# Kernel optimization log

Measured on AMD Instinct MI355X. Metric: run time of the kernel, lower is better.

Reference implementation:

```python
import jax, jax.numpy as jnp
import numpy as np
from jax import lax

PATCH = 7
SIGMA = 12.0


def _pairwise_patch_dist_sq(A, B, p):
    # A: (Na, C, H, W), B: (Nb, C, H, W)
    # squared diff of every image pair, summed over channels -> (Na, Nb, H, W)
    diff_sq = ((A[:, None] - B[None, :]) ** 2).sum(axis=2)
    Na, Nb, H, W = diff_sq.shape
    x = diff_sq.reshape(Na * Nb, 1, H, W)
    k = jnp.ones((1, 1, p, p), dtype=x.dtype)  # box filter == conv2d with ones kernel
    d = lax.conv_general_dilated(x, k, window_strides=(1, 1), padding='VALID')
    return d.reshape(Na, Nb, H - p + 1, W - p + 1)


def _kernel_mean(d_sq, sigma, exclude_diagonal):
    K = jnp.exp(-d_sq / (2.0 * sigma ** 2))  # Gaussian RBF on squared distances
    K_pair = K.mean(axis=(-2, -1))            # (Na, Nb)
    if exclude_diagonal:
        n = K_pair.shape[0]
        off = jnp.float32(1.0) - jnp.eye(n, dtype=K_pair.dtype)
        return (K_pair * off).sum() / (n * (n - 1))
    return K_pair.mean()


def setup_inputs() -> dict:
    key = jax.random.key(0)
    kx, ky = jax.random.split(key)
    x = jax.random.normal(kx, (64, 3, 64, 64), dtype=jnp.float32)
    y = jax.random.normal(ky, (64, 3, 64, 64), dtype=jnp.float32)
    return {"x": x, "y": y}


def reference(x, y):
    d_xx = _pairwise_patch_dist_sq(x, x, PATCH)
    d_yy = _pairwise_patch_dist_sq(y, y, PATCH)
    d_xy = _pairwise_patch_dist_sq(x, y, PATCH)
    return (_kernel_mean(d_xx, SIGMA, True)
            - 2.0 * _kernel_mean(d_xy, SIGMA, False)
            + _kernel_mean(d_yy, SIGMA, True))
```

## Files before the change

kernel.cpp:

```cpp
#include <hip/hip_runtime.h>

#define NIMG 64
#define CH 3
#define WW 64
#define PLANE 4096
#define IMGSZ (CH * PLANE)
#define HO 58
#define WO 58
#define NSLOT 64

#define DS 68
#define HS 68
#define DOFF 0
#define HOFF (64 * DS)

__global__ __launch_bounds__(256) void patchmmd_pair_kernel(
    const float* __restrict__ x, const float* __restrict__ y,
    double* __restrict__ acc)
{
    const int i = blockIdx.x, j = blockIdx.y, z = blockIdx.z;
    if (z < 2 && i >= j) return;

    const float* __restrict__ A = ((z == 1) ? y : x) + (size_t)i * IMGSZ;
    const float* __restrict__ B = ((z == 0) ? x : y) + (size_t)j * IMGSZ;

    __shared__ __align__(16) float lds[HOFF + 64 * HS + 16];

    const int tid = threadIdx.x;

    #pragma unroll
    for (int t = 0; t < 4; ++t) {
        const int v = tid + t * 256;
        const int r = v >> 4, q = v & 15;
        const int off = r * WW + q * 4;
        float4 d = make_float4(0.f, 0.f, 0.f, 0.f);
        #pragma unroll
        for (int ch = 0; ch < CH; ++ch) {
            const float4 av = *reinterpret_cast<const float4*>(A + ch * PLANE + off);
            const float4 bv = *reinterpret_cast<const float4*>(B + ch * PLANE + off);
            const float ex = av.x - bv.x, ey = av.y - bv.y,
                        ez = av.z - bv.z, ew = av.w - bv.w;
            d.x = fmaf(ex, ex, d.x); d.y = fmaf(ey, ey, d.y);
            d.z = fmaf(ez, ez, d.z); d.w = fmaf(ew, ew, d.w);
        }
        *reinterpret_cast<float4*>(&lds[DOFF + r * DS + q * 4]) = d;
    }
    __syncthreads();

    #pragma unroll
    for (int t = 0; t < 2; ++t) {
        const int v = tid + t * 256;
        const int r = v >> 3, s = v & 7;
        const float* src = &lds[DOFF + r * DS + s * 8];
        const float4 q0 = *reinterpret_cast<const float4*>(src);
        const float4 q1 = *reinterpret_cast<const float4*>(src + 4);
        const float4 q2 = *reinterpret_cast<const float4*>(src + 8);
        const float4 q3 = *reinterpret_cast<const float4*>(src + 12);
        const float d0=q0.x,d1=q0.y,d2=q0.z,d3=q0.w, d4=q1.x,d5=q1.y,d6=q1.z,d7=q1.w,
                    d8=q2.x,d9=q2.y,d10=q2.z,d11=q2.w, d12=q3.x,d13=q3.y;
        float h0 = d0+d1+d2+d3+d4+d5+d6;
        const float h1 = h0 + d7  - d0;
        const float h2 = h1 + d8  - d1;
        const float h3 = h2 + d9  - d2;
        const float h4 = h3 + d10 - d3;
        const float h5 = h4 + d11 - d4;
        const float h6 = h5 + d12 - d5;
        const float h7 = h6 + d13 - d6;
        float* dst = &lds[HOFF + r * HS + s * 8];
        *reinterpret_cast<float4*>(dst)     = make_float4(h0, h1, h2, h3);
        *reinterpret_cast<float4*>(dst + 4) = make_float4(h4, h5, h6, h7);
    }
    __syncthreads();

    const float NEG_INV_2S2 = -1.0f / 288.0f;
    float local = 0.f;
    #pragma unroll
    for (int t = 0; t < 2; ++t) {
        const int v = tid + t * 256;
        const int c = v & 63;
        const int g = v >> 6;
        float hr[14];
        #pragma unroll
        for (int k = 0; k < 14; ++k) {
            const int rk = min(8 * g + k, 63);
            hr[k] = lds[HOFF + rk * HS + c];
        }
        float V = hr[0]+hr[1]+hr[2]+hr[3]+hr[4]+hr[5]+hr[6];
        #pragma unroll
        for (int jj = 0; jj < 8; ++jj) {
            if (jj > 0) V += hr[jj + 6] - hr[jj - 1];
            if ((8 * g + jj) < HO && c < WO)
                local += __expf(V * NEG_INV_2S2);
        }
    }

    #pragma unroll
    for (int off = 32; off; off >>= 1)
        local += __shfl_down(local, off, 64);
    __syncthreads();
    if ((tid & 63) == 0) lds[tid >> 6] = local;
    __syncthreads();
    if (tid == 0) {
        const float tot = lds[0] + lds[1] + lds[2] + lds[3];
        const int slot = z * NSLOT + ((i ^ (j * 19)) & (NSLOT - 1));
        atomicAdd(&acc[slot], (double)tot);
    }
}

__global__ void patchmmd_combine_kernel(const double* __restrict__ acc,
                                        float* __restrict__ out)
{
    double s[3] = {0.0, 0.0, 0.0};
    for (int z = 0; z < 3; ++z)
        for (int k = 0; k < NSLOT; ++k) s[z] += acc[z * NSLOT + k];
    const double inv_hw = 1.0 / (double)(HO * WO);
    const double mean_xx = 2.0 * s[0] * inv_hw / (64.0 * 63.0);
    const double mean_yy = 2.0 * s[1] * inv_hw / (64.0 * 63.0);
    const double mean_xy = s[2] * inv_hw / (64.0 * 64.0);
    out[0] = (float)(mean_xx - 2.0 * mean_xy + mean_yy);
}

extern "C" void kernel_launch(void* const* d_in, const int* in_sizes, int n_in,
                              void* d_out, int out_size, void* d_ws, size_t ws_size,
                              hipStream_t stream)
{
    const float* x = (const float*)d_in[0];
    const float* y = (const float*)d_in[1];
    float* out  = (float*)d_out;
    double* acc = (double*)d_ws;

    hipMemsetAsync(acc, 0, 3 * NSLOT * sizeof(double), stream);

    dim3 grid(NIMG, NIMG, 3);
    patchmmd_pair_kernel<<<grid, 256, 0, stream>>>(x, y, acc);
    patchmmd_combine_kernel<<<1, 1, 0, stream>>>(acc, out);
}
```

Baseline: 96.31 us.

## Fuse diff-square and horizontal box sum in registers, parallelize combine reduction

Each thread now loads 16 contiguous columns of one row for all channels and computes the squared differences and the horizontal 7-wide sliding sum in registers. It fetches the 6 neighbour values it needs from the adjacent lane with shuffles, which removes the intermediate LDS buffer and one barrier. The final combine kernel now runs with 64 threads and reduces with wavefront shuffles instead of a serial loop. The trade-offs are higher register pressure and less coalesced global loads, since each thread reads strided float4 chunks.

```diff
diff --git a/kernel.cpp b/kernel.cpp
--- a/kernel.cpp
+++ b/kernel.cpp
@@ -8,11 +8,7 @@
 #define HO 58
 #define WO 58
 #define NSLOT 64
-
-#define DS 68
 #define HS 68
-#define DOFF 0
-#define HOFF (64 * DS)
 
 __global__ __launch_bounds__(256) void patchmmd_pair_kernel(
     const float* __restrict__ x, const float* __restrict__ y,
@@ -24,51 +20,73 @@
     const float* __restrict__ A = ((z == 1) ? y : x) + (size_t)i * IMGSZ;
     const float* __restrict__ B = ((z == 0) ? x : y) + (size_t)j * IMGSZ;
 
-    __shared__ __align__(16) float lds[HOFF + 64 * HS + 16];
+    __shared__ __align__(16) float Hs[64 * HS + 16];
+    __shared__ float wsum[4];
 
     const int tid = threadIdx.x;
 
-    #pragma unroll
-    for (int t = 0; t < 4; ++t) {
-        const int v = tid + t * 256;
-        const int r = v >> 4, q = v & 15;
-        const int off = r * WW + q * 4;
-        float4 d = make_float4(0.f, 0.f, 0.f, 0.f);
+    {
+        const int r = tid >> 2;
+        const int s = tid & 3;
+        const int c0 = s * 16;
+        const int base = r * WW + c0;
+
+        float4 qa[6], qb[6];
         #pragma unroll
         for (int ch = 0; ch < CH; ++ch) {
-            const float4 av = *reinterpret_cast<const float4*>(A + ch * PLANE + off);
-            const float4 bv = *reinterpret_cast<const float4*>(B + ch * PLANE + off);
-            const float ex = av.x - bv.x, ey = av.y - bv.y,
-                        ez = av.z - bv.z, ew = av.w - bv.w;
-            d.x = fmaf(ex, ex, d.x); d.y = fmaf(ey, ey, d.y);
-            d.z = fmaf(ez, ez, d.z); d.w = fmaf(ew, ew, d.w);
+            #pragma unroll
+            for (int q = 0; q < 2; ++q) {
+                qa[ch * 2 + q] = *reinterpret_cast<const float4*>(A + ch * PLANE + base + q * 8);
+                qb[ch * 2 + q] = *reinterpret_cast<const float4*>(B + ch * PLANE + base + q * 8);
+            }
         }
-        *reinterpret_cast<float4*>(&lds[DOFF + r * DS + q * 4]) = d;
-    }
-    __syncthreads();
+        float4 qa2[6], qb2[6];
+        #pragma unroll
+        for (int ch = 0; ch < CH; ++ch) {
+            #pragma unroll
+            for (int q = 0; q < 2; ++q) {
+                qa2[ch * 2 + q] = *reinterpret_cast<const float4*>(A + ch * PLANE + base + 4 + q * 8);
+                qb2[ch * 2 + q] = *reinterpret_cast<const float4*>(B + ch * PLANE + base + 4 + q * 8);
+            }
+        }
 
-    #pragma unroll
-    for (int t = 0; t < 2; ++t) {
-        const int v = tid + t * 256;
-        const int r = v >> 3, s = v & 7;
-        const float* src = &lds[DOFF + r * DS + s * 8];
-        const float4 q0 = *reinterpret_cast<const float4*>(src);
-        const float4 q1 = *reinterpret_cast<const float4*>(src + 4);
-        const float4 q2 = *reinterpret_cast<const float4*>(src + 8);
-        const float4 q3 = *reinterpret_cast<const float4*>(src + 12);
-        const float d0=q0.x,d1=q0.y,d2=q0.z,d3=q0.w, d4=q1.x,d5=q1.y,d6=q1.z,d7=q1.w,
-                    d8=q2.x,d9=q2.y,d10=q2.z,d11=q2.w, d12=q3.x,d13=q3.y;
-        float h0 = d0+d1+d2+d3+d4+d5+d6;
-        const float h1 = h0 + d7  - d0;
-        const float h2 = h1 + d8  - d1;
-        const float h3 = h2 + d9  - d2;
-        const float h4 = h3 + d10 - d3;
-        const float h5 = h4 + d11 - d4;
-        const float h6 = h5 + d12 - d5;
-        const float h7 = h6 + d13 - d6;
-        float* dst = &lds[HOFF + r * HS + s * 8];
-        *reinterpret_cast<float4*>(dst)     = make_float4(h0, h1, h2, h3);
-        *reinterpret_cast<float4*>(dst + 4) = make_float4(h4, h5, h6, h7);
+        float d[16];
+        #pragma unroll
+        for (int k = 0; k < 16; ++k) d[k] = 0.f;
+        #pragma unroll
+        for (int ch = 0; ch < CH; ++ch) {
+            #pragma unroll
+            for (int q = 0; q < 2; ++q) {
+                const float4 av = qa[ch * 2 + q],  bv = qb[ch * 2 + q];
+                const float4 aw = qa2[ch * 2 + q], bw = qb2[ch * 2 + q];
+                float e;
+                e = av.x - bv.x; d[q * 8 + 0] = fmaf(e, e, d[q * 8 + 0]);
+                e = av.y - bv.y; d[q * 8 + 1] = fmaf(e, e, d[q * 8 + 1]);
+                e = av.z - bv.z; d[q * 8 + 2] = fmaf(e, e, d[q * 8 + 2]);
+                e = av.w - bv.w; d[q * 8 + 3] = fmaf(e, e, d[q * 8 + 3]);
+                e = aw.x - bw.x; d[q * 8 + 4] = fmaf(e, e, d[q * 8 + 4]);
+                e = aw.y - bw.y; d[q * 8 + 5] = fmaf(e, e, d[q * 8 + 5]);
+                e = aw.z - bw.z; d[q * 8 + 6] = fmaf(e, e, d[q * 8 + 6]);
+                e = aw.w - bw.w; d[q * 8 + 7] = fmaf(e, e, d[q * 8 + 7]);
+            }
+        }
+
+        float dn[6];
+        #pragma unroll
+        for (int m = 0; m < 6; ++m) dn[m] = __shfl_down(d[m], 1, 64);
+
+        float h[16];
+        h[0] = d[0] + d[1] + d[2] + d[3] + d[4] + d[5] + d[6];
+        #pragma unroll
+        for (int k = 1; k < 10; ++k)  h[k] = h[k - 1] + d[k + 6]      - d[k - 1];
+        #pragma unroll
+        for (int k = 10; k < 16; ++k) h[k] = h[k - 1] + dn[k - 10]    - d[k - 1];
+
+        float* dst = &Hs[r * HS + c0];
+        *reinterpret_cast<float4*>(dst)      = make_float4(h[0],  h[1],  h[2],  h[3]);
+        *reinterpret_cast<float4*>(dst + 4)  = make_float4(h[4],  h[5],  h[6],  h[7]);
+        *reinterpret_cast<float4*>(dst + 8)  = make_float4(h[8],  h[9],  h[10], h[11]);
+        *reinterpret_cast<float4*>(dst + 12) = make_float4(h[12], h[13], h[14], h[15]);
     }
     __syncthreads();
 
@@ -83,7 +101,7 @@
         #pragma unroll
         for (int k = 0; k < 14; ++k) {
             const int rk = min(8 * g + k, 63);
-            hr[k] = lds[HOFF + rk * HS + c];
+            hr[k] = Hs[rk * HS + c];
         }
         float V = hr[0]+hr[1]+hr[2]+hr[3]+hr[4]+hr[5]+hr[6];
         #pragma unroll
@@ -97,11 +115,10 @@
     #pragma unroll
     for (int off = 32; off; off >>= 1)
         local += __shfl_down(local, off, 64);
-    __syncthreads();
-    if ((tid & 63) == 0) lds[tid >> 6] = local;
+    if ((tid & 63) == 0) wsum[tid >> 6] = local;
     __syncthreads();
     if (tid == 0) {
-        const float tot = lds[0] + lds[1] + lds[2] + lds[3];
+        const float tot = wsum[0] + wsum[1] + wsum[2] + wsum[3];
         const int slot = z * NSLOT + ((i ^ (j * 19)) & (NSLOT - 1));
         atomicAdd(&acc[slot], (double)tot);
     }
@@ -110,14 +127,23 @@
 __global__ void patchmmd_combine_kernel(const double* __restrict__ acc,
                                         float* __restrict__ out)
 {
-    double s[3] = {0.0, 0.0, 0.0};
-    for (int z = 0; z < 3; ++z)
-        for (int k = 0; k < NSLOT; ++k) s[z] += acc[z * NSLOT + k];
-    const double inv_hw = 1.0 / (double)(HO * WO);
-    const double mean_xx = 2.0 * s[0] * inv_hw / (64.0 * 63.0);
-    const double mean_yy = 2.0 * s[1] * inv_hw / (64.0 * 63.0);
-    const double mean_xy = s[2] * inv_hw / (64.0 * 64.0);
-    out[0] = (float)(mean_xx - 2.0 * mean_xy + mean_yy);
+    const int lane = threadIdx.x;
+    double s0 = acc[0 * NSLOT + lane];
+    double s1 = acc[1 * NSLOT + lane];
+    double s2 = acc[2 * NSLOT + lane];
+    #pragma unroll
+    for (int off = 32; off; off >>= 1) {
+        s0 += __shfl_down(s0, off, 64);
+        s1 += __shfl_down(s1, off, 64);
+        s2 += __shfl_down(s2, off, 64);
+    }
+    if (lane == 0) {
+        const double inv_hw = 1.0 / (double)(HO * WO);
+        const double mean_xx = 2.0 * s0 * inv_hw / (64.0 * 63.0);
+        const double mean_yy = 2.0 * s1 * inv_hw / (64.0 * 63.0);
+        const double mean_xy = s2 * inv_hw / (64.0 * 64.0);
+        out[0] = (float)(mean_xx - 2.0 * mean_xy + mean_yy);
+    }
 }
 
 extern "C" void kernel_launch(void* const* d_in, const int* in_sizes, int n_in,
@@ -133,5 +159,5 @@
 
     dim3 grid(NIMG, NIMG, 3);
     patchmmd_pair_kernel<<<grid, 256, 0, stream>>>(x, y, acc);
-    patchmmd_combine_kernel<<<1, 1, 0, stream>>>(acc, out);
+    patchmmd_combine_kernel<<<1, 64, 0, stream>>>(acc, out);
 }
```

After: 122.8 us. 27.5% more time.
